# Optimization experiments

Measured on AMD Instinct MI355X. Metric: run time of the kernel, lower is better.

## Reference

```python
import jax, jax.numpy as jnp
import numpy as np
from jax import lax

B, D, BOND, OUT = 16384, 784, 5, 10

def setup_inputs() -> dict:
    key = jax.random.key(0)
    k = jax.random.split(key, 6)
    x = jax.random.uniform(k[0], (B, D), dtype=jnp.float32)
    core_first = jax.random.normal(k[1], (1, 2, BOND), dtype=jnp.float32) * 0.1
    cores_mid = jax.random.normal(k[2], (D - 2, BOND, 2, BOND), dtype=jnp.float32) * 0.1
    core_last = jax.random.normal(k[3], (BOND, 2, 1), dtype=jnp.float32) * 0.1
    # xavier_uniform for fc.weight with fan_in=1, fan_out=OUT
    bound = float(np.sqrt(6.0 / (1 + OUT)))
    fc_w = jax.random.uniform(k[4], (OUT, 1), dtype=jnp.float32, minval=-bound, maxval=bound)
    fc_b = jnp.zeros((OUT,), dtype=jnp.float32)
    return {"x": x, "core_first": core_first, "cores_mid": cores_mid,
            "core_last": core_last, "fc_w": fc_w, "fc_b": fc_b}

def reference(x, core_first, cores_mid, core_last, fc_w, fc_b):
    # x: [B, D] -> feature map [B, D, 2] = stack(1-x, x)
    xs = jnp.stack([1.0 - x, x], axis=-1)            # [B, D, 2]
    # first core: (1, 2, bond) -> initial carry [B, bond]
    carry0 = jnp.einsum('bi,ir->br', xs[:, 0], core_first[0])  # [B, bond]
    # sequential tensor-train contraction over middle sites via scan
    xs_mid = jnp.moveaxis(xs[:, 1:-1], 1, 0)          # [D-2, B, 2]
    def step(carry, inp):
        xi, core = inp                                # xi: [B,2], core: [bond,2,bond]
        carry = jnp.einsum('bl,bi,lir->br', carry, xi, core)
        return carry, None
    carry, _ = lax.scan(step, carry0, (xs_mid, cores_mid))
    # last core: (bond, 2, 1) -> scalar per batch element
    vlast = jnp.einsum('bi,li->bl', xs[:, -1], core_last[:, :, 0])  # [B, bond]
    res = jnp.sum(carry * vlast, axis=-1, keepdims=True)            # [B, 1]
    out = res @ fc_w.T + fc_b                          # [B, OUT]
    return out
```

## Files before the change

### kernel.cpp

```cpp
#include <hip/hip_runtime.h>


constexpr int Bn     = 16384;
constexpr int Dn     = 784;
constexpr int NOUT   = 10;
constexpr int NPAIR  = 390;
constexpr int PKP    = 100;
constexpr int BWD_P0 = 375;

__global__ void prepack_pairs(const float* __restrict__ cm, float* __restrict__ pk)
{
    int idx = blockIdx.x * 256 + threadIdx.x;
    if (idx >= NPAIR * 100) return;
    int p = idx / 100, rest = idx - p * 100;
    int q = rest / 25, e = rest - q * 25;
    int l = e / 5, r = e - l * 5;
    int m1 = 2 * p + 1, m2 = 2 * p + 2;
    const float* L = cm + (size_t)(m1 * 5 + l) * 10;
    float acc = 0.f;
#pragma unroll
    for (int k = 0; k < 5; ++k) {
        float Lk = (q & 1) ? (L[5 + k] - L[k]) : L[k];
        const float* R = cm + (size_t)(m2 * 5 + k) * 10;
        float Rk = (q & 2) ? (R[5 + r] - R[r]) : R[r];
        acc = fmaf(Lk, Rk, acc);
    }
    int wl = l, wr = r;
    if (p >= BWD_P0) { wl = r; wr = l; }
    pk[(size_t)p * PKP + q * 25 + wl * 5 + wr] = acc;
}

__device__ __forceinline__ void buildC(const float* __restrict__ s,
                                       float xa, float xb, float C[25]) {
    const float xab = xa * xb;
#pragma unroll
    for (int k = 0; k < 25; ++k) {
        float t = xab * s[75 + k];
        t = fmaf(xb, s[50 + k], t);
        t = fmaf(xa, s[25 + k], t);
        C[k] = t + s[k];
    }
}

__device__ __forceinline__ void vstep(float c[5], const float C[25]) {
    float t[5];
#pragma unroll
    for (int r = 0; r < 5; ++r) t[r] = c[0] * C[r];
#pragma unroll
    for (int l = 1; l < 5; ++l)
#pragma unroll
        for (int r = 0; r < 5; ++r) t[r] = fmaf(c[l], C[l * 5 + r], t[r]);
#pragma unroll
    for (int r = 0; r < 5; ++r) c[r] = t[r];
}

__device__ __forceinline__ void mstep(float M[25], const float C[25]) {
#pragma unroll
    for (int i = 0; i < 5; ++i) {
        float t[5];
#pragma unroll
        for (int r = 0; r < 5; ++r) t[r] = M[i * 5] * C[r];
#pragma unroll
        for (int l = 1; l < 5; ++l)
#pragma unroll
            for (int r = 0; r < 5; ++r) t[r] = fmaf(M[i * 5 + l], C[l * 5 + r], t[r]);
#pragma unroll
        for (int r = 0; r < 5; ++r) M[i * 5 + r] = t[r];
    }
}

__global__ __launch_bounds__(1024, 4)
void mps_half_kernel(const float* __restrict__ x,
                     const float* __restrict__ core_first,
                     const float* __restrict__ cores_mid,
                     const float* __restrict__ core_last,
                     const float* __restrict__ pk,
                     float* __restrict__ out)
{
    __shared__ float matbuf[8][25][64];

    const int lane = threadIdx.x & 63;
    const int wseg = __builtin_amdgcn_readfirstlane(threadIdx.x >> 6);
    const int half = blockIdx.x & 1;
    const int row  = (blockIdx.x >> 1) * 64 + lane;
    const float*  __restrict__ xr  = x + (size_t)row * Dn;
    const float2* __restrict__ xr2 = (const float2*)xr;

    const bool isVec = (half == 0) ? (wseg == 0) : (wseg == 15);

    float M[25];
    float cl[5];
    float C[25];

    if (!isVec) {
        const int p0 = (half == 0) ? (15 + 12 * (wseg - 1)) : (195 + 12 * wseg);
        const float* __restrict__ s = pk + (size_t)p0 * PKP;
#pragma unroll
        for (int k = 0; k < 25; ++k) M[k] = (k % 6 == 0) ? 1.0f : 0.0f;
#pragma unroll 1
        for (int i = 0; i < 12; ++i) {
            const float2 xv = xr2[p0 + i + 1];
            buildC(s, xv.x, xv.y, C);
            mstep(M, C);
            s += PKP;
        }
    } else if (half == 0) {
        const float2 x01 = xr2[0];
        float cn[5];
#pragma unroll
        for (int r = 0; r < 5; ++r)
            cl[r] = fmaf(x01.x, core_first[5 + r] - core_first[r], core_first[r]);
        const float* cm0 = cores_mid;
#pragma unroll
        for (int r = 0; r < 5; ++r) {
            float a = 0.f;
#pragma unroll
            for (int l = 0; l < 5; ++l) {
                float mm = fmaf(x01.y, cm0[l * 10 + 5 + r] - cm0[l * 10 + r],
                                cm0[l * 10 + r]);
                a = fmaf(cl[l], mm, a);
            }
            cn[r] = a;
        }
#pragma unroll
        for (int r = 0; r < 5; ++r) cl[r] = cn[r];
        const float* __restrict__ s = pk;
#pragma unroll 1
        for (int p = 0; p < 15; ++p) {
            const float2 xv = xr2[p + 1];
            buildC(s, xv.x, xv.y, C);
            vstep(cl, C);
            s += PKP;
        }
    } else {
        const float2 xz = xr2[391];
        float vl[5], vn[5];
#pragma unroll
        for (int l = 0; l < 5; ++l)
            vl[l] = fmaf(xz.y, core_last[2 * l + 1] - core_last[2 * l],
                         core_last[2 * l]);
        const float* cmL = cores_mid + (size_t)781 * 50;
#pragma unroll
        for (int l = 0; l < 5; ++l) {
            float a = 0.f;
#pragma unroll
            for (int r = 0; r < 5; ++r) {
                float mm = fmaf(xz.x, cmL[l * 10 + 5 + r] - cmL[l * 10 + r],
                                cmL[l * 10 + r]);
                a = fmaf(mm, vl[r], a);
            }
            vn[l] = a;
        }
#pragma unroll
        for (int l = 0; l < 5; ++l) cl[l] = vn[l];
        const float* __restrict__ s = pk + (size_t)(NPAIR - 1) * PKP;
#pragma unroll 1
        for (int p = NPAIR - 1; p >= BWD_P0; --p) {
            const float2 xv = xr2[p + 1];
            buildC(s, xv.x, xv.y, C);
            vstep(cl, C);
            s -= PKP;
        }
    }

    if (!isVec && ((half == 0 && wseg <= 8) || (half == 1 && wseg >= 8))) {
        const int slot = (half == 0) ? (wseg - 1) : (wseg - 8);
#pragma unroll
        for (int k = 0; k < 25; ++k) matbuf[slot][k][lane] = M[k];
    }
    __syncthreads();

    if (isVec) {
        if (half == 0) {
#pragma unroll 1
            for (int s2 = 0; s2 < 8; ++s2) {
                float t[5];
#pragma unroll
                for (int r = 0; r < 5; ++r) t[r] = cl[0] * matbuf[s2][r][lane];
#pragma unroll
                for (int l = 1; l < 5; ++l)
#pragma unroll
                    for (int r = 0; r < 5; ++r)
                        t[r] = fmaf(cl[l], matbuf[s2][l * 5 + r][lane], t[r]);
#pragma unroll
                for (int r = 0; r < 5; ++r) cl[r] = t[r];
            }
        } else {
#pragma unroll 1
            for (int s2 = 6; s2 >= 0; --s2) {
                float t[5];
#pragma unroll
                for (int l = 0; l < 5; ++l) {
                    float a = matbuf[s2][l * 5][lane] * cl[0];
#pragma unroll
                    for (int r = 1; r < 5; ++r)
                        a = fmaf(matbuf[s2][l * 5 + r][lane], cl[r], a);
                    t[l] = a;
                }
#pragma unroll
                for (int l = 0; l < 5; ++l) cl[l] = t[l];
            }
        }
    }
    __syncthreads();

    if (!isVec && ((half == 0 && wseg >= 9) || (half == 1 && wseg <= 7))) {
        const int slot = (half == 0) ? (wseg - 9) : wseg;
#pragma unroll
        for (int k = 0; k < 25; ++k) matbuf[slot][k][lane] = M[k];
    }
    __syncthreads();

    if (isVec) {
        float* orow = out + (size_t)row * NOUT;
        if (half == 0) {
#pragma unroll 1
            for (int s2 = 0; s2 < 7; ++s2) {
                float t[5];
#pragma unroll
                for (int r = 0; r < 5; ++r) t[r] = cl[0] * matbuf[s2][r][lane];
#pragma unroll
                for (int l = 1; l < 5; ++l)
#pragma unroll
                    for (int r = 0; r < 5; ++r)
                        t[r] = fmaf(cl[l], matbuf[s2][l * 5 + r][lane], t[r]);
#pragma unroll
                for (int r = 0; r < 5; ++r) cl[r] = t[r];
            }
#pragma unroll
            for (int i = 0; i < 5; ++i) orow[i] = cl[i];
        } else {
#pragma unroll 1
            for (int s2 = 7; s2 >= 0; --s2) {
                float t[5];
#pragma unroll
                for (int l = 0; l < 5; ++l) {
                    float a = matbuf[s2][l * 5][lane] * cl[0];
#pragma unroll
                    for (int r = 1; r < 5; ++r)
                        a = fmaf(matbuf[s2][l * 5 + r][lane], cl[r], a);
                    t[l] = a;
                }
#pragma unroll
                for (int l = 0; l < 5; ++l) cl[l] = t[l];
            }
#pragma unroll
            for (int i = 0; i < 5; ++i) orow[5 + i] = cl[i];
        }
    }
}

__global__ __launch_bounds__(256)
void finalize_kernel(const float* __restrict__ fc_w, const float* __restrict__ fc_b,
                     float* __restrict__ out)
{
    const int row = blockIdx.x * 256 + threadIdx.x;
    float* o = out + (size_t)row * NOUT;
    float f[5], g[5];
#pragma unroll
    for (int i = 0; i < 5; ++i) { f[i] = o[i]; g[i] = o[5 + i]; }
    float res = f[0] * g[0];
#pragma unroll
    for (int i = 1; i < 5; ++i) res = fmaf(f[i], g[i], res);
#pragma unroll
    for (int k = 0; k < NOUT; ++k) o[k] = fmaf(res, fc_w[k], fc_b[k]);
}

extern "C" void kernel_launch(void* const* d_in, const int* in_sizes, int n_in,
                              void* d_out, int out_size, void* d_ws, size_t ws_size,
                              hipStream_t stream) {
    const float* x          = (const float*)d_in[0];
    const float* core_first = (const float*)d_in[1];
    const float* cores_mid  = (const float*)d_in[2];
    const float* core_last  = (const float*)d_in[3];
    const float* fc_w       = (const float*)d_in[4];
    const float* fc_b       = (const float*)d_in[5];
    float* out              = (float*)d_out;
    float* pk               = (float*)d_ws;

    hipLaunchKernelGGL(prepack_pairs, dim3((NPAIR * 100 + 255) / 256), dim3(256),
                       0, stream, cores_mid, pk);
    hipLaunchKernelGGL(mps_half_kernel, dim3(Bn / 64 * 2), dim3(1024), 0, stream,
                       x, core_first, cores_mid, core_last, pk, out);
    hipLaunchKernelGGL(finalize_kernel, dim3(Bn / 256), dim3(256), 0, stream,
                       fc_w, fc_b, out);
}
```

Baseline: 141.0 us.

## Halve waves per block, lengthen per-wave segments, drop two-phase shared reduction

Each block half now uses 8 waves instead of 16. Each matrix wave multiplies 22 pair-matrices instead of 12, and the vector waves run 41 and 41 pairs instead of 15 and 16. All seven matrix products fit in shared memory at once, so the two-stage write, combine and barrier sequence becomes a single write followed by one combine pass. This removes two barriers and half the matrix-matrix work, whose 5x5 products cost five times a vector step. In exchange each wave has a longer serial chain and fewer waves are resident to hide latency.

```diff
diff --git a/kernel.cpp b/kernel.cpp
--- a/kernel.cpp
+++ b/kernel.cpp
@@ -6,7 +6,9 @@
 constexpr int NOUT   = 10;
 constexpr int NPAIR  = 390;
 constexpr int PKP    = 100;
-constexpr int BWD_P0 = 375;
+constexpr int BWD_P0 = 349;
+constexpr int VECP   = 41;
+constexpr int MATP   = 22;
 
 __global__ void prepack_pairs(const float* __restrict__ cm, float* __restrict__ pk)
 {
@@ -69,7 +71,7 @@
     }
 }
 
-__global__ __launch_bounds__(1024, 4)
+__global__ __launch_bounds__(512, 4)
 void mps_half_kernel(const float* __restrict__ x,
                      const float* __restrict__ core_first,
                      const float* __restrict__ cores_mid,
@@ -77,7 +79,7 @@
                      const float* __restrict__ pk,
                      float* __restrict__ out)
 {
-    __shared__ float matbuf[8][25][64];
+    __shared__ float matbuf[7][25][64];
 
     const int lane = threadIdx.x & 63;
     const int wseg = __builtin_amdgcn_readfirstlane(threadIdx.x >> 6);
@@ -86,24 +88,28 @@
     const float*  __restrict__ xr  = x + (size_t)row * Dn;
     const float2* __restrict__ xr2 = (const float2*)xr;
 
-    const bool isVec = (half == 0) ? (wseg == 0) : (wseg == 15);
+    const bool isVec = (half == 0) ? (wseg == 0) : (wseg == 7);
 
     float M[25];
     float cl[5];
     float C[25];
 
     if (!isVec) {
-        const int p0 = (half == 0) ? (15 + 12 * (wseg - 1)) : (195 + 12 * wseg);
+        const int p0 = (half == 0) ? (VECP + MATP * (wseg - 1))
+                                   : (195 + MATP * wseg);
         const float* __restrict__ s = pk + (size_t)p0 * PKP;
 #pragma unroll
         for (int k = 0; k < 25; ++k) M[k] = (k % 6 == 0) ? 1.0f : 0.0f;
 #pragma unroll 1
-        for (int i = 0; i < 12; ++i) {
+        for (int i = 0; i < MATP; ++i) {
             const float2 xv = xr2[p0 + i + 1];
             buildC(s, xv.x, xv.y, C);
             mstep(M, C);
             s += PKP;
         }
+        const int slot = (half == 0) ? (wseg - 1) : wseg;
+#pragma unroll
+        for (int k = 0; k < 25; ++k) matbuf[slot][k][lane] = M[k];
     } else if (half == 0) {
         const float2 x01 = xr2[0];
         float cn[5];
@@ -126,7 +132,7 @@
         for (int r = 0; r < 5; ++r) cl[r] = cn[r];
         const float* __restrict__ s = pk;
 #pragma unroll 1
-        for (int p = 0; p < 15; ++p) {
+        for (int p = 0; p < VECP; ++p) {
             const float2 xv = xr2[p + 1];
             buildC(s, xv.x, xv.y, C);
             vstep(cl, C);
@@ -163,52 +169,6 @@
         }
     }
 
-    if (!isVec && ((half == 0 && wseg <= 8) || (half == 1 && wseg >= 8))) {
-        const int slot = (half == 0) ? (wseg - 1) : (wseg - 8);
-#pragma unroll
-        for (int k = 0; k < 25; ++k) matbuf[slot][k][lane] = M[k];
-    }
-    __syncthreads();
-
-    if (isVec) {
-        if (half == 0) {
-#pragma unroll 1
-            for (int s2 = 0; s2 < 8; ++s2) {
-                float t[5];
-#pragma unroll
-                for (int r = 0; r < 5; ++r) t[r] = cl[0] * matbuf[s2][r][lane];
-#pragma unroll
-                for (int l = 1; l < 5; ++l)
-#pragma unroll
-                    for (int r = 0; r < 5; ++r)
-                        t[r] = fmaf(cl[l], matbuf[s2][l * 5 + r][lane], t[r]);
-#pragma unroll
-                for (int r = 0; r < 5; ++r) cl[r] = t[r];
-            }
-        } else {
-#pragma unroll 1
-            for (int s2 = 6; s2 >= 0; --s2) {
-                float t[5];
-#pragma unroll
-                for (int l = 0; l < 5; ++l) {
-                    float a = matbuf[s2][l * 5][lane] * cl[0];
-#pragma unroll
-                    for (int r = 1; r < 5; ++r)
-                        a = fmaf(matbuf[s2][l * 5 + r][lane], cl[r], a);
-                    t[l] = a;
-                }
-#pragma unroll
-                for (int l = 0; l < 5; ++l) cl[l] = t[l];
-            }
-        }
-    }
-    __syncthreads();
-
-    if (!isVec && ((half == 0 && wseg >= 9) || (half == 1 && wseg <= 7))) {
-        const int slot = (half == 0) ? (wseg - 9) : wseg;
-#pragma unroll
-        for (int k = 0; k < 25; ++k) matbuf[slot][k][lane] = M[k];
-    }
     __syncthreads();
 
     if (isVec) {
@@ -231,7 +191,7 @@
             for (int i = 0; i < 5; ++i) orow[i] = cl[i];
         } else {
 #pragma unroll 1
-            for (int s2 = 7; s2 >= 0; --s2) {
+            for (int s2 = 6; s2 >= 0; --s2) {
                 float t[5];
 #pragma unroll
                 for (int l = 0; l < 5; ++l) {
@@ -280,7 +240,7 @@
 
     hipLaunchKernelGGL(prepack_pairs, dim3((NPAIR * 100 + 255) / 256), dim3(256),
                        0, stream, cores_mid, pk);
-    hipLaunchKernelGGL(mps_half_kernel, dim3(Bn / 64 * 2), dim3(1024), 0, stream,
+    hipLaunchKernelGGL(mps_half_kernel, dim3(Bn / 64 * 2), dim3(512), 0, stream,
                        x, core_first, cores_mid, core_last, pk, out);
     hipLaunchKernelGGL(finalize_kernel, dim3(Bn / 256), dim3(256), 0, stream,
                        fc_w, fc_b, out);
```

Result: slower. 150.0 us (+6.4%).
